# Kernel tuning notes

Hardware: AMD Instinct MI355X
Metric: run time of the kernel (lower is better)

Reference implementation:

```python
import jax, jax.numpy as jnp
import numpy as np
from jax import lax


def setup_inputs() -> dict:
    key = jax.random.key(0)
    k1, k2, k3, k4 = jax.random.split(key, 4)
    H = 2048
    L = 3
    hidden_states = jax.random.normal(k1, (2, 4096, H), dtype=jnp.float32)
    Win = jax.random.normal(k2, (3 * H, H), dtype=jnp.float32) * (H ** -0.5)
    conv_w = jax.random.normal(k3, (H, 1, L), dtype=jnp.float32) * (L ** -0.5)
    Wout = jax.random.normal(k4, (H, H), dtype=jnp.float32) * (H ** -0.5)
    return {"hidden_states": hidden_states, "Win": Win, "conv_w": conv_w, "Wout": Wout}


def reference(hidden_states, Win, conv_w, Wout):
    H = hidden_states.shape[-1]
    L = conv_w.shape[-1]
    BCx = jnp.einsum('bsh,oh->bso', hidden_states, Win)  # (b, s, 3H)
    B, C, x = jnp.split(BCx, 3, axis=-1)
    Bx = jnp.transpose(B * x, (0, 2, 1))  # (b, H, s)
    # depthwise causal conv: left-pad L-1 so output length == s (torch pads both
    # sides then slices [..., :seqlen]; left-only padding is equivalent)
    conv_out = lax.conv_general_dilated(
        Bx, conv_w, window_strides=(1,), padding=[(L - 1, 0)],
        feature_group_count=H, dimension_numbers=('NCH', 'OIH', 'NCH'))
    y = C * jnp.transpose(conv_out, (0, 2, 1))  # (b, s, H)
    return jnp.einsum('bsh,oh->bso', y, Wout)
```

## Files before the change

kernel.cpp:

```cpp
#include <hip/hip_runtime.h>
#include <hip/hip_bf16.h>

typedef unsigned short u16;
typedef __attribute__((ext_vector_type(8))) short bf16x8;
typedef __attribute__((ext_vector_type(4))) float f32x4;

static __device__ __forceinline__ u16 f2bf(float f) {
    unsigned u = __float_as_uint(f);
    unsigned r = (u + 0x7fffu + ((u >> 16) & 1u)) >> 16;
    return (u16)r;
}
static __device__ __forceinline__ float bf2f(u16 u) {
    return __uint_as_float(((unsigned)u) << 16);
}

static __device__ __forceinline__ void async_copy16(const void* gptr, void* lptr) {
    __builtin_amdgcn_global_load_lds(
        (const __attribute__((address_space(1))) void*)gptr,
        (__attribute__((address_space(3))) void*)lptr, 16, 0, 0);
}

__global__ __launch_bounds__(256)
void cvt_all(const float* __restrict__ a, const float* __restrict__ b,
             const float* __restrict__ c,
             u16* __restrict__ oa, u16* __restrict__ ob, u16* __restrict__ oc) {
    int blk = blockIdx.x;
    const float* src; u16* dst; long base;
    if (blk < 16384)      { src = a; dst = oa; base = blk; }
    else if (blk < 28672) { src = b; dst = ob; base = blk - 16384; }
    else                  { src = c; dst = oc; base = blk - 28672; }
    long i = (base * 256 + threadIdx.x) * 4;
    float4 f = *(const float4*)(src + i);
    u16 o[4] = { f2bf(f.x), f2bf(f.y), f2bf(f.z), f2bf(f.w) };
    *(uint2*)(dst + i) = *(const uint2*)o;
}

template<bool BF16_OUT>
__global__ __launch_bounds__(512, 2)
void gemm_bt8(const u16* __restrict__ A, const u16* __restrict__ B,
              void* __restrict__ Cout, int M, int N, int K) {
    __shared__ __align__(16) u16 lds[65536];

    const int t    = threadIdx.x;
    const int lane = t & 63;
    const int wm   = (t >> 6) >> 2;
    const int wn   = (t >> 6) & 3;
    const int l15  = lane & 15;
    const int hi   = lane >> 4;
    const int l7   = lane & 7;

    const int id   = blockIdx.y * gridDim.x + blockIdx.x;
    const int cpx  = gridDim.x >> 3;
    const int bx   = (id & 7) * cpx + ((id >> 3) % cpx);
    const int by   = (id >> 3) / cpx;
    const long rowA = (long)by * 256;
    const long rowB = (long)bx * 256;

    const int pl0 = t >> 3;
    const int slotcol = ((t & 7) ^ (pl0 & 7)) * 8;
    const u16* Asrc[2][2]; const u16* Bsrc[2][2];
#pragma unroll
    for (int h = 0; h < 2; h++) {
        int gA0 = h * 64 + pl0;
        int gA1 = 128 + h * 64 + pl0;
        Asrc[h][0] = A + (rowA + gA0) * K + slotcol;
        Asrc[h][1] = A + (rowA + gA1) * K + slotcol;
        int nB0 = (pl0 >> 5) * 64 + h * 32 + (pl0 & 31);
        int nB1 = ((64 + pl0) >> 5) * 64 + h * 32 + (pl0 & 31);
        Bsrc[h][0] = B + (rowB + nB0) * K + slotcol;
        Bsrc[h][1] = B + (rowB + nB1) * K + slotcol;
    }
    const int t8 = t * 8;

    auto STAGE = [&](int bufo, bool isB, int h, int kk) {
        const u16* s0 = (isB ? Bsrc : Asrc)[h][0] + kk;
        const u16* s1 = (isB ? Bsrc : Asrc)[h][1] + kk;
        u16* d = lds + bufo + (isB ? 16384 : 0) + h * 8192 + t8;
        async_copy16(s0, d);
        async_copy16(s1, d + 4096);
    };

    const int aBase = wm * 4096 + l15 * 64;
    const int bBase = 16384 + wn * 2048 + l15 * 64;
    const int sOff0 = (hi ^ l7) * 8;
    const int sOff1 = ((4 + hi) ^ l7) * 8;

    bf16x8 af[4][2], bg0[2][2], bg1[2][2];
    f32x4 acc[8][4] = {};

    auto LOAD_AF = [&](int bufo, int Mq) {
#pragma unroll
        for (int m = 0; m < 4; m++) {
            const u16* p = lds + bufo + Mq * 8192 + aBase + m * 1024;
            af[m][0] = *(const bf16x8*)(p + sOff0);
            af[m][1] = *(const bf16x8*)(p + sOff1);
        }
    };
    auto LOAD_BG = [&](int bufo, int Nq, bf16x8 (*bg)[2]) {
#pragma unroll
        for (int n = 0; n < 2; n++) {
            const u16* p = lds + bufo + Nq * 8192 + bBase + n * 1024;
            bg[n][0] = *(const bf16x8*)(p + sOff0);
            bg[n][1] = *(const bf16x8*)(p + sOff1);
        }
    };
    auto MFMA_Q = [&](int Mq, int Nq, bf16x8 (*bg)[2]) {
        __builtin_amdgcn_s_setprio(1);
#pragma unroll
        for (int ks = 0; ks < 2; ks++)
#pragma unroll
            for (int m = 0; m < 4; m++)
#pragma unroll
                for (int n = 0; n < 2; n++)
                    acc[Mq * 4 + m][Nq * 2 + n] =
                        __builtin_amdgcn_mfma_f32_16x16x32_bf16(
                            af[m][ks], bg[n][ks], acc[Mq * 4 + m][Nq * 2 + n],
                            0, 0, 0);
        __builtin_amdgcn_s_setprio(0);
    };

#define BAR()   __builtin_amdgcn_s_barrier()
#define WAITL() do { asm volatile("s_waitcnt lgkmcnt(0)" ::: "memory"); \
                     __builtin_amdgcn_sched_barrier(0); } while (0)
#define VM6()   asm volatile("s_waitcnt vmcnt(6)" ::: "memory")

    STAGE(0, false, 0, 0);  STAGE(0, false, 1, 0);
    STAGE(0, true,  0, 0);  STAGE(0, true,  1, 0);
    STAGE(32768, false, 0, 64);
    STAGE(32768, true,  0, 64);  STAGE(32768, true, 1, 64);
    VM6();
    BAR();

#pragma unroll 1
    for (int k0 = 0; k0 < K; k0 += 128) {
        int kN1 = k0 + 64;
        int kN2 = k0 + 128; if (kN2 >= K) kN2 = 0;
        int kN3 = k0 + 192; if (kN3 >= K) kN3 -= K;
        LOAD_AF(0, 0); LOAD_BG(0, 0, bg0);
        STAGE(32768, false, 1, kN1);
        BAR(); WAITL();
        MFMA_Q(0, 0, bg0); BAR();
        LOAD_BG(0, 1, bg1);
        STAGE(0, false, 0, kN2);
        BAR(); WAITL();
        MFMA_Q(0, 1, bg1); BAR();
        LOAD_AF(0, 1);
        STAGE(0, true, 0, kN2);
        BAR(); WAITL();
        MFMA_Q(1, 0, bg0); BAR();
        STAGE(0, true, 1, kN2);
        VM6();
        BAR();
        MFMA_Q(1, 1, bg1); BAR();
        LOAD_AF(32768, 0); LOAD_BG(32768, 0, bg0);
        STAGE(0, false, 1, kN2);
        BAR(); WAITL();
        MFMA_Q(0, 0, bg0); BAR();
        LOAD_BG(32768, 1, bg1);
        STAGE(32768, false, 0, kN3);
        BAR(); WAITL();
        MFMA_Q(0, 1, bg1); BAR();
        LOAD_AF(32768, 1);
        STAGE(32768, true, 0, kN3);
        BAR(); WAITL();
        MFMA_Q(1, 0, bg0); BAR();
        STAGE(32768, true, 1, kN3);
        VM6();
        BAR();
        MFMA_Q(1, 1, bg1); BAR();
    }
    asm volatile("s_waitcnt vmcnt(0)" ::: "memory");

#undef BAR
#undef WAITL
#undef VM6

    const long crowBase = rowA + wm * 128 + hi * 4;
    const long ccolBase = rowB + wn * 64 + l15;
#pragma unroll
    for (int mi = 0; mi < 8; mi++) {
#pragma unroll
        for (int nj = 0; nj < 4; nj++) {
            long base = (crowBase + mi * 16) * N + ccolBase + nj * 16;
#pragma unroll
            for (int r = 0; r < 4; r++) {
                float v = acc[mi][nj][r];
                long idx = base + (long)r * N;
                if (BF16_OUT) ((u16*)Cout)[idx] = f2bf(v);
                else          ((float*)Cout)[idx] = v;
            }
        }
    }
}

union U16x8 { uint4 v; u16 u[8]; };

__global__ __launch_bounds__(256)
void conv_fuse(const u16* __restrict__ BCx, const float* __restrict__ cw,
               u16* __restrict__ y) {
    const int row = blockIdx.x;
    const int h0  = threadIdx.x * 8;
    const int sl  = row & 4095;
    const u16* r0 = BCx + (long)row * 6144;

    U16x8 B0, X0, C0, B1, X1, B2, X2;
    B0.v = *(const uint4*)(r0 + h0);
    C0.v = *(const uint4*)(r0 + 2048 + h0);
    X0.v = *(const uint4*)(r0 + 4096 + h0);
    if (sl >= 1) {
        B1.v = *(const uint4*)(r0 - 6144 + h0);
        X1.v = *(const uint4*)(r0 - 6144 + 4096 + h0);
    } else { B1.v = make_uint4(0,0,0,0); X1.v = make_uint4(0,0,0,0); }
    if (sl >= 2) {
        B2.v = *(const uint4*)(r0 - 12288 + h0);
        X2.v = *(const uint4*)(r0 - 12288 + 4096 + h0);
    } else { B2.v = make_uint4(0,0,0,0); X2.v = make_uint4(0,0,0,0); }

    U16x8 o;
#pragma unroll
    for (int i = 0; i < 8; i++) {
        int h = h0 + i;
        float bx0 = bf2f(B0.u[i]) * bf2f(X0.u[i]);
        float bx1 = bf2f(B1.u[i]) * bf2f(X1.u[i]);
        float bx2 = bf2f(B2.u[i]) * bf2f(X2.u[i]);
        float v = cw[h*3+2] * bx0 + cw[h*3+1] * bx1 + cw[h*3] * bx2;
        o.u[i] = f2bf(v * bf2f(C0.u[i]));
    }
    *(uint4*)(y + (long)row * 2048 + h0) = o.v;
}

extern "C" void kernel_launch(void* const* d_in, const int* in_sizes, int n_in,
                              void* d_out, int out_size, void* d_ws, size_t ws_size,
                              hipStream_t stream) {
    const float* hs   = (const float*)d_in[0];
    const float* Win  = (const float*)d_in[1];
    const float* cw   = (const float*)d_in[2];
    const float* Wout = (const float*)d_in[3];
    float* out = (float*)d_out;

    char* ws = (char*)d_ws;
    u16* hsb   = (u16*)(ws);
    u16* Winb  = (u16*)(ws +  33554432);
    u16* Woutb = (u16*)(ws +  58720256);
    u16* bcx   = (u16*)(ws +  67108864);
    u16* yb    = (u16*)(ws + 167772160);

    cvt_all<<<32768, 256, 0, stream>>>(hs, Win, Wout, hsb, Winb, Woutb);

    gemm_bt8<true ><<<dim3(24, 32), 512, 0, stream>>>(hsb, Winb, bcx, 8192, 6144, 2048);

    conv_fuse<<<8192, 256, 0, stream>>>(bcx, cw, yb);

    gemm_bt8<false><<<dim3(8, 32), 512, 0, stream>>>(yb, Woutb, out, 8192, 2048, 2048);
}
```

Before: 437.0 us.

## Restructure GEMM main loop into finer-grained LDS/MFMA interleaved pipeline

Rewrites the bf16 GEMM inner loop so each 64-wide K tile is processed as a macro that splits A-fragment LDS reads into halves and waits on partial lgkmcnt, letting MFMAs start before all fragments arrive. Global-to-LDS staging for the next tile is issued per quadrant with adjusted vmcnt waits, and barriers around each quadrant are reduced. Quadrant order is changed to reuse B fragments across A halves. It also fixes B row indexing to a simple +128 offset and adds 64-bit stride casts. The risk is subtle race conditions on the double buffer and different register pressure.

Measured after the change: 432.9 us. No clear change (-0.9%).

```diff
diff --git a/kernel.cpp b/kernel.cpp
--- a/kernel.cpp
+++ b/kernel.cpp
@@ -63,21 +63,23 @@
     for (int h = 0; h < 2; h++) {
         int gA0 = h * 64 + pl0;
         int gA1 = 128 + h * 64 + pl0;
-        Asrc[h][0] = A + (rowA + gA0) * K + slotcol;
-        Asrc[h][1] = A + (rowA + gA1) * K + slotcol;
+        Asrc[h][0] = A + (rowA + gA0) * (long)K + slotcol;
+        Asrc[h][1] = A + (rowA + gA1) * (long)K + slotcol;
         int nB0 = (pl0 >> 5) * 64 + h * 32 + (pl0 & 31);
-        int nB1 = ((64 + pl0) >> 5) * 64 + h * 32 + (pl0 & 31);
-        Bsrc[h][0] = B + (rowB + nB0) * K + slotcol;
-        Bsrc[h][1] = B + (rowB + nB1) * K + slotcol;
+        Bsrc[h][0] = B + (rowB + nB0) * (long)K + slotcol;
+        Bsrc[h][1] = B + (rowB + nB0 + 128) * (long)K + slotcol;
     }
     const int t8 = t * 8;
 
-    auto STAGE = [&](int bufo, bool isB, int h, int kk) {
-        const u16* s0 = (isB ? Bsrc : Asrc)[h][0] + kk;
-        const u16* s1 = (isB ? Bsrc : Asrc)[h][1] + kk;
-        u16* d = lds + bufo + (isB ? 16384 : 0) + h * 8192 + t8;
-        async_copy16(s0, d);
-        async_copy16(s1, d + 4096);
+    auto STAGE_A = [&](int bufo, int h, int kk) {
+        u16* d = lds + bufo + h * 8192 + t8;
+        async_copy16(Asrc[h][0] + kk, d);
+        async_copy16(Asrc[h][1] + kk, d + 4096);
+    };
+    auto STAGE_B = [&](int bufo, int h, int kk) {
+        u16* d = lds + bufo + 16384 + h * 8192 + t8;
+        async_copy16(Bsrc[h][0] + kk, d);
+        async_copy16(Bsrc[h][1] + kk, d + 4096);
     };
 
     const int aBase = wm * 4096 + l15 * 64;
@@ -85,31 +87,29 @@
     const int sOff0 = (hi ^ l7) * 8;
     const int sOff1 = ((4 + hi) ^ l7) * 8;
 
-    bf16x8 af[4][2], bg0[2][2], bg1[2][2];
+    bf16x8 af[4][2], ba[2][2], bb[2][2];
     f32x4 acc[8][4] = {};
 
-    auto LOAD_AF = [&](int bufo, int Mq) {
-#pragma unroll
-        for (int m = 0; m < 4; m++) {
-            const u16* p = lds + bufo + Mq * 8192 + aBase + m * 1024;
-            af[m][0] = *(const bf16x8*)(p + sOff0);
-            af[m][1] = *(const bf16x8*)(p + sOff1);
-        }
-    };
-    auto LOAD_BG = [&](int bufo, int Nq, bf16x8 (*bg)[2]) {
-#pragma unroll
-        for (int n = 0; n < 2; n++) {
-            const u16* p = lds + bufo + Nq * 8192 + bBase + n * 1024;
-            bg[n][0] = *(const bf16x8*)(p + sOff0);
-            bg[n][1] = *(const bf16x8*)(p + sOff1);
-        }
-    };
-    auto MFMA_Q = [&](int Mq, int Nq, bf16x8 (*bg)[2]) {
+    auto LOAD_A2 = [&](int bufo, int Mq, int mb) {
+        const u16* p = lds + bufo + Mq * 8192 + aBase + mb * 1024;
+        af[mb][0]     = *(const bf16x8*)(p + sOff0);
+        af[mb][1]     = *(const bf16x8*)(p + sOff1);
+        af[mb + 1][0] = *(const bf16x8*)(p + 1024 + sOff0);
+        af[mb + 1][1] = *(const bf16x8*)(p + 1024 + sOff1);
+    };
+    auto LOAD_B = [&](bf16x8 (&bg)[2][2], int bufo, int Nq) {
+        const u16* p = lds + bufo + Nq * 8192 + bBase;
+        bg[0][0] = *(const bf16x8*)(p + sOff0);
+        bg[0][1] = *(const bf16x8*)(p + sOff1);
+        bg[1][0] = *(const bf16x8*)(p + 1024 + sOff0);
+        bg[1][1] = *(const bf16x8*)(p + 1024 + sOff1);
+    };
+    auto MFMA_H = [&](int Mq, int Nq, int mb, bf16x8 (&bg)[2][2]) {
         __builtin_amdgcn_s_setprio(1);
 #pragma unroll
         for (int ks = 0; ks < 2; ks++)
 #pragma unroll
-            for (int m = 0; m < 4; m++)
+            for (int m = mb; m < mb + 2; m++)
 #pragma unroll
                 for (int n = 0; n < 2; n++)
                     acc[Mq * 4 + m][Nq * 2 + n] =
@@ -120,60 +120,48 @@
     };
 
 #define BAR()   __builtin_amdgcn_s_barrier()
-#define WAITL() do { asm volatile("s_waitcnt lgkmcnt(0)" ::: "memory"); \
+#define SB()    __builtin_amdgcn_sched_barrier(0)
+#define LGKM(n) do { asm volatile("s_waitcnt lgkmcnt(" #n ")" ::: "memory"); \
                      __builtin_amdgcn_sched_barrier(0); } while (0)
-#define VM6()   asm volatile("s_waitcnt vmcnt(6)" ::: "memory")
-
-    STAGE(0, false, 0, 0);  STAGE(0, false, 1, 0);
-    STAGE(0, true,  0, 0);  STAGE(0, true,  1, 0);
-    STAGE(32768, false, 0, 64);
-    STAGE(32768, true,  0, 64);  STAGE(32768, true, 1, 64);
-    VM6();
+#define VM(n)   asm volatile("s_waitcnt vmcnt(" #n ")" ::: "memory")
+
+#define TILE(BC, BN, KK)                                                     \
+                                                              \
+    LOAD_B(ba, BC, 0); LOAD_A2(BC, 0, 0); SB(); LOAD_A2(BC, 0, 2);           \
+    STAGE_A(BN, 0, KK); VM(2);                                               \
+    LGKM(4); MFMA_H(0, 0, 0, ba); LGKM(0); MFMA_H(0, 0, 2, ba); BAR();       \
+                                                              \
+    LOAD_B(bb, BC, 1);                                                       \
+    STAGE_B(BN, 0, KK);                                                      \
+    LGKM(0); MFMA_H(0, 1, 0, bb); MFMA_H(0, 1, 2, bb); BAR();                \
+                                                              \
+    LOAD_A2(BC, 1, 0); SB(); LOAD_A2(BC, 1, 2);                              \
+    STAGE_A(BN, 1, KK);                                                      \
+    LGKM(4); MFMA_H(1, 1, 0, bb); LGKM(0); MFMA_H(1, 1, 2, bb); BAR();       \
+                                                              \
+    STAGE_B(BN, 1, KK); VM(4);                                               \
+    MFMA_H(1, 0, 0, ba); MFMA_H(1, 0, 2, ba); BAR();
+
+    STAGE_A(0, 0, 0);  STAGE_B(0, 0, 0);
+    STAGE_A(0, 1, 0);  STAGE_B(0, 1, 0);
+    asm volatile("s_waitcnt vmcnt(0)" ::: "memory");
     BAR();
 
+    const int NT = K >> 6;
 #pragma unroll 1
-    for (int k0 = 0; k0 < K; k0 += 128) {
-        int kN1 = k0 + 64;
-        int kN2 = k0 + 128; if (kN2 >= K) kN2 = 0;
-        int kN3 = k0 + 192; if (kN3 >= K) kN3 -= K;
-        LOAD_AF(0, 0); LOAD_BG(0, 0, bg0);
-        STAGE(32768, false, 1, kN1);
-        BAR(); WAITL();
-        MFMA_Q(0, 0, bg0); BAR();
-        LOAD_BG(0, 1, bg1);
-        STAGE(0, false, 0, kN2);
-        BAR(); WAITL();
-        MFMA_Q(0, 1, bg1); BAR();
-        LOAD_AF(0, 1);
-        STAGE(0, true, 0, kN2);
-        BAR(); WAITL();
-        MFMA_Q(1, 0, bg0); BAR();
-        STAGE(0, true, 1, kN2);
-        VM6();
-        BAR();
-        MFMA_Q(1, 1, bg1); BAR();
-        LOAD_AF(32768, 0); LOAD_BG(32768, 0, bg0);
-        STAGE(0, false, 1, kN2);
-        BAR(); WAITL();
-        MFMA_Q(0, 0, bg0); BAR();
-        LOAD_BG(32768, 1, bg1);
-        STAGE(32768, false, 0, kN3);
-        BAR(); WAITL();
-        MFMA_Q(0, 1, bg1); BAR();
-        LOAD_AF(32768, 1);
-        STAGE(32768, true, 0, kN3);
-        BAR(); WAITL();
-        MFMA_Q(1, 0, bg0); BAR();
-        STAGE(32768, true, 1, kN3);
-        VM6();
-        BAR();
-        MFMA_Q(1, 1, bg1); BAR();
-    }
-    asm volatile("s_waitcnt vmcnt(0)" ::: "memory");
-
+    for (int i = 0; i < NT; i += 2) {
+        int k1 = (i + 1) << 6;
+        int k2 = (i + 2 < NT) ? (i + 2) << 6 : 0;
+        TILE(0, 32768, k1);
+        TILE(32768, 0, k2);
+    }
+    asm volatile("s_waitcnt vmcnt(0) lgkmcnt(0)" ::: "memory");
+
+#undef TILE
+#undef VM
+#undef LGKM
+#undef SB
 #undef BAR
-#undef WAITL
-#undef VM6
 
     const long crowBase = rowA + wm * 128 + hi * 4;
     const long ccolBase = rowB + wn * 64 + l15;
```
